# Kernel tuning notes

Measured on AMD Instinct MI355X. Metric: run time of the kernel, lower is better.

## Reference

```python
import jax, jax.numpy as jnp
import numpy as np

K = 3          # kernel size
KF = K * K     # kernel field = 9
PAD = 1
STRIDE = 1


def _conv(x, w, b):
    y = jax.lax.conv_general_dilated(
        x, w, (STRIDE, STRIDE), [(PAD, PAD), (PAD, PAD)],
        dimension_numbers=('NCHW', 'OIHW', 'NCHW'))
    return y + b[None, :, None, None]


def _bilinear_gather(x, py, px):
    # x: [B,C,H,W]; py/px: [B,KF,Ho,Wo] float sampling coords (zero-pad outside)
    B, C, H, W = x.shape
    xf = x.reshape(B, C, H * W)
    y0 = jnp.floor(py)
    x0 = jnp.floor(px)

    def corner(yc, xc):
        wy = 1.0 - jnp.abs(py - yc)
        wx = 1.0 - jnp.abs(px - xc)
        valid = (yc >= 0) & (yc <= H - 1) & (xc >= 0) & (xc <= W - 1)
        yi = jnp.clip(yc, 0, H - 1).astype(jnp.int32)
        xi = jnp.clip(xc, 0, W - 1).astype(jnp.int32)
        idx = (yi * W + xi).reshape(B, -1)               # [B, KF*Ho*Wo]
        v = jax.vmap(lambda f, i: f[:, i])(xf, idx)      # [B, C, KF*Ho*Wo]
        wgt = (wy * wx * valid.astype(x.dtype)).reshape(B, 1, -1)
        return v * wgt

    return (corner(y0, x0) + corner(y0, x0 + 1) +
            corner(y0 + 1, x0) + corner(y0 + 1, x0 + 1))  # [B,C,KF*Ho*Wo]


def _deform_conv(x, offset, mask, w, b):
    # modulated deformable conv v2 (mmcv offset layout: [y,x] interleaved per kernel pt)
    B, C, H, W = x.shape
    Ho, Wo = mask.shape[2], mask.shape[3]
    kh, kw = jnp.meshgrid(jnp.arange(K), jnp.arange(K), indexing='ij')
    kh = kh.reshape(-1).astype(x.dtype)   # [KF]
    kw = kw.reshape(-1).astype(x.dtype)
    base_y = (jnp.arange(Ho) * STRIDE - PAD).astype(x.dtype)
    base_x = (jnp.arange(Wo) * STRIDE - PAD).astype(x.dtype)
    off = offset.reshape(B, KF, 2, Ho, Wo)
    py = base_y[None, None, :, None] + kh[None, :, None, None] + off[:, :, 0]
    px = base_x[None, None, None, :] + kw[None, :, None, None] + off[:, :, 1]
    val = _bilinear_gather(x, py, px).reshape(B, C, KF, Ho, Wo)
    val = val * mask[:, None]                             # modulate
    out = jnp.einsum('bckhw,ock->bohw', val, w.reshape(w.shape[0], C, KF))
    return out + b[None, :, None, None]


def setup_inputs() -> dict:
    key = jax.random.key(0)
    k1, k2, k3 = jax.random.split(key, 3)
    B, C, H, W = 8, 64, 128, 128
    x = jax.random.normal(k1, (B, C, H, W), dtype=jnp.float32)
    w_om = jax.random.normal(k2, (3 * KF, C, K, K), dtype=jnp.float32) * 0.02
    b_om = jnp.zeros((3 * KF,), dtype=jnp.float32)
    w_dc = jax.random.normal(k3, (64, C, K, K), dtype=jnp.float32) * 0.05
    b_dc = jnp.zeros((64,), dtype=jnp.float32)
    return {"x": x, "w_om": w_om, "b_om": b_om, "w_dc": w_dc, "b_dc": b_dc}


def reference(x, w_om, b_om, w_dc, b_dc):
    om = _conv(x, w_om, b_om)                 # [B, 3*KF, H, W]
    offset = om[:, :2 * KF]
    mask = 2.0 * jax.nn.sigmoid(om[:, 2 * KF:])
    return _deform_conv(x, offset, mask, w_dc, b_dc)
```

## Files before the change

### kernel.cpp

```cpp
#include <hip/hip_runtime.h>
#include <cmath>

#define IH 128
#define IW 128
#define NB 8

typedef __attribute__((ext_vector_type(8))) short bf16x8;
typedef __attribute__((ext_vector_type(4))) float f32x4;

union U4B8 { uint4 u; bf16x8 h; };

#define XT_OFF   0
#define WTDC_OFF 4194304
#define WTOM_OFF (4194304 + 18432)

__device__ __forceinline__ unsigned short f32_to_bf16(float f) {
    unsigned int u = __float_as_uint(f);
    u += 0x7fffu + ((u >> 16) & 1u);
    return (unsigned short)(u >> 16);
}

__global__ void transpose_weights(const float* __restrict__ w_dc,
                                  const float* __restrict__ w_om,
                                  unsigned short* __restrict__ wt_dc16,
                                  unsigned short* __restrict__ wt_om16) {
    int idx = blockIdx.x * blockDim.x + threadIdx.x;
    if (idx < 9 * 64 * 64) {
        int k = idx >> 12;
        int o = (idx >> 6) & 63;
        int c = idx & 63;
        wt_dc16[idx] = f32_to_bf16(w_dc[(o * 64 + c) * 9 + k]);
    }
    if (idx < 9 * 32 * 64) {
        int k = idx >> 11;
        int o = (idx >> 6) & 31;
        int c = idx & 63;
        wt_om16[idx] = (o < 27) ? f32_to_bf16(w_om[(o * 64 + c) * 9 + k])
                                : (unsigned short)0;
    }
}

__global__ __launch_bounds__(256) void transpose_x(
        const float* __restrict__ x, unsigned short* __restrict__ xT) {
    __shared__ float t[64 * 65];
    const int tid = threadIdx.x;
    const int blk = blockIdx.x;
    const int b = blk >> 8;
    const int rem = blk & 255;
    const int h = rem >> 1;
    const int w0 = (rem & 1) << 6;

    for (int i = tid; i < 4096; i += 256) {
        const int c = i >> 6;
        const int w = i & 63;
        t[w * 65 + c] = x[(((size_t)(b * 64 + c)) << 14) + (h << 7) + w0 + w];
    }
    __syncthreads();
    const int c2 = (tid & 31) * 2;
    ushort2* dst = (ushort2*)(xT + (((size_t)b << 20)) + ((size_t)((h << 7) + w0)) * 64 + c2);
#pragma unroll
    for (int p = 0; p < 8; ++p) {
        const int w = (tid >> 5) + p * 8;
        ushort2 u;
        u.x = f32_to_bf16(t[w * 65 + c2]);
        u.y = f32_to_bf16(t[w * 65 + c2 + 1]);
        dst[(size_t)w * 32] = u;
    }
}

__device__ __forceinline__ void corner2(const unsigned short* __restrict__ p,
                                        float wgt, float* v) {
    const uint4 a = *(const uint4*)p;
    const uint4 c = *(const uint4*)(p + 32);
    unsigned int u[8] = {a.x, a.y, a.z, a.w, c.x, c.y, c.z, c.w};
#pragma unroll
    for (int i = 0; i < 8; ++i) {
        v[2 * i]     += wgt * __uint_as_float(u[i] << 16);
        v[2 * i + 1] += wgt * __uint_as_float(u[i] & 0xffff0000u);
    }
}

__global__ __launch_bounds__(256, 2) void fused_dcn(
        const unsigned short* __restrict__ xT,
        const float* __restrict__ b_om,
        const unsigned short* __restrict__ wt_om16,
        const float* __restrict__ b_dc,
        const unsigned short* __restrict__ wt_dc16,
        float* __restrict__ out) {
    __shared__ __align__(16) unsigned short wall[9 * 8 * 64 * 8];
    __shared__ __align__(16) float offs[27 * 68];

    const int tid = threadIdx.x;
    const int b = blockIdx.x >> 8;
    const int rem = blockIdx.x & 255;
    const int h = rem >> 1;
    const int w0 = (rem & 1) << 6;
    const int wid = tid >> 6;
    const int lane = tid & 63;
    const int ln15 = lane & 15;
    const int quad = lane >> 4;

    const unsigned short* xb = xT + ((size_t)b << 20);

    for (int s = tid; s < 2304; s += 256) {
        const int k = s >> 8;
        const int r = s & 255;
        const int p = r >> 5;
        const int o = r & 31;
        ((uint4*)wall)[s] = ((const uint4*)wt_om16)[(k << 8) + (o << 3) + p];
    }
    __syncthreads();

    {
        f32x4 acc[2] = {{0.f, 0.f, 0.f, 0.f}, {0.f, 0.f, 0.f, 0.f}};
#pragma unroll
        for (int k = 0; k < 9; ++k) {
            const int kh = k / 3;
            const int kw = k - kh * 3;
            const int y = h + kh - 1;
            const int xx = w0 + (wid << 4) + ln15 + kw - 1;
            U4B8 a0, a1;
            a0.u = make_uint4(0u, 0u, 0u, 0u);
            a1.u = make_uint4(0u, 0u, 0u, 0u);
            if (y >= 0 && y < IH && xx >= 0 && xx < IW) {
                const unsigned short* p = xb + (((size_t)((y << 7) + xx)) << 6) + (quad << 3);
                a0.u = *(const uint4*)p;
                a1.u = *(const uint4*)(p + 32);
            }
            const unsigned short* wb  = wall + (((k << 3) + quad) << 8);
            const unsigned short* wb4 = wall + (((k << 3) + quad + 4) << 8);
#pragma unroll
            for (int ot = 0; ot < 2; ++ot) {
                U4B8 b0, b1;
                b0.u = *(const uint4*)&wb [((ot << 4) + ln15) << 3];
                b1.u = *(const uint4*)&wb4[((ot << 4) + ln15) << 3];
                acc[ot] = __builtin_amdgcn_mfma_f32_16x16x32_bf16(a0.h, b0.h, acc[ot], 0, 0, 0);
                acc[ot] = __builtin_amdgcn_mfma_f32_16x16x32_bf16(a1.h, b1.h, acc[ot], 0, 0, 0);
            }
        }
#pragma unroll
        for (int ot = 0; ot < 2; ++ot) {
            const int o = (ot << 4) + ln15;
            if (o < 27) {
                const float bias = b_om[o];
                float4 r;
                r.x = acc[ot][0] + bias;
                r.y = acc[ot][1] + bias;
                r.z = acc[ot][2] + bias;
                r.w = acc[ot][3] + bias;
                if (o >= 18) {
                    r.x = 2.0f / (1.0f + __expf(-r.x));
                    r.y = 2.0f / (1.0f + __expf(-r.y));
                    r.z = 2.0f / (1.0f + __expf(-r.z));
                    r.w = 2.0f / (1.0f + __expf(-r.w));
                }
                *(float4*)&offs[o * 68 + (wid << 4) + (quad << 2)] = r;
            }
        }
    }
    __syncthreads();

    for (int s = tid; s < 4608; s += 256) {
        const int k = s >> 9;
        const int r = s & 511;
        const int p = r >> 6;
        const int o = r & 63;
        ((uint4*)wall)[s] = ((const uint4*)wt_dc16)[(k << 9) + (o << 3) + p];
    }
    __syncthreads();

    const int lpx = (wid << 4) + ln15;

    f32x4 acc[4];
#pragma unroll
    for (int i = 0; i < 4; ++i) acc[i] = (f32x4){0.f, 0.f, 0.f, 0.f};

#pragma unroll
    for (int k = 0; k < 9; ++k) {
        const float offy = offs[(2 * k) * 68 + lpx];
        const float offx = offs[(2 * k + 1) * 68 + lpx];
        const float msk  = offs[(18 + k) * 68 + lpx];
        const int kh = k / 3;
        const int kw = k - kh * 3;
        const float py  = (float)(h + kh - 1) + offy;
        const float pxf = (float)(w0 + lpx + kw - 1) + offx;
        const float y0f = floorf(py);
        const float x0f = floorf(pxf);
        const float fy = py - y0f;
        const float fx = pxf - x0f;
        const float wy0 = 1.0f - fy, wx0 = 1.0f - fx;
        const float vy0 = (y0f >= 0.0f && y0f <= 127.0f) ? 1.0f : 0.0f;
        const float vy1 = (y0f >= -1.0f && y0f <= 126.0f) ? 1.0f : 0.0f;
        const float vx0 = (x0f >= 0.0f && x0f <= 127.0f) ? 1.0f : 0.0f;
        const float vx1 = (x0f >= -1.0f && x0f <= 126.0f) ? 1.0f : 0.0f;
        const float w00 = wy0 * wx0 * vy0 * vx0;
        const float w01 = wy0 * fx  * vy0 * vx1;
        const float w10 = fy  * wx0 * vy1 * vx0;
        const float w11 = fy  * fx  * vy1 * vx1;
        const int y0i = min(max((int)y0f, 0), 127);
        const int y1i = min(max((int)y0f + 1, 0), 127);
        const int x0i = min(max((int)x0f, 0), 127);
        const int x1i = min(max((int)x0f + 1, 0), 127);

        float v[16];
#pragma unroll
        for (int i = 0; i < 16; ++i) v[i] = 0.0f;
        const int cofs = quad << 3;
        corner2(xb + ((((size_t)((y0i << 7) + x0i)) << 6) + cofs), w00, v);
        corner2(xb + ((((size_t)((y0i << 7) + x1i)) << 6) + cofs), w01, v);
        corner2(xb + ((((size_t)((y1i << 7) + x0i)) << 6) + cofs), w10, v);
        corner2(xb + ((((size_t)((y1i << 7) + x1i)) << 6) + cofs), w11, v);

        U4B8 a0, a1;
        unsigned int pk[8];
#pragma unroll
        for (int i = 0; i < 8; ++i) {
            const unsigned int lo = f32_to_bf16(v[2 * i] * msk);
            const unsigned int hi = f32_to_bf16(v[2 * i + 1] * msk);
            pk[i] = lo | (hi << 16);
        }
        a0.u = make_uint4(pk[0], pk[1], pk[2], pk[3]);
        a1.u = make_uint4(pk[4], pk[5], pk[6], pk[7]);

        const unsigned short* wb  = wall + (((k << 3) + quad) << 9);
        const unsigned short* wb4 = wall + (((k << 3) + quad + 4) << 9);
#pragma unroll
        for (int ot = 0; ot < 4; ++ot) {
            U4B8 b0, b1;
            b0.u = *(const uint4*)&wb [((ot << 4) + ln15) << 3];
            b1.u = *(const uint4*)&wb4[((ot << 4) + ln15) << 3];
            acc[ot] = __builtin_amdgcn_mfma_f32_16x16x32_bf16(a0.h, b0.h, acc[ot], 0, 0, 0);
            acc[ot] = __builtin_amdgcn_mfma_f32_16x16x32_bf16(a1.h, b1.h, acc[ot], 0, 0, 0);
        }
    }

#pragma unroll
    for (int ot = 0; ot < 4; ++ot) {
        const int o = (ot << 4) + ln15;
        const float bias = b_dc[o];
        float4 r;
        r.x = acc[ot][0] + bias;
        r.y = acc[ot][1] + bias;
        r.z = acc[ot][2] + bias;
        r.w = acc[ot][3] + bias;
        *(float4*)&out[(((size_t)(b * 64 + o)) << 14) + (h << 7) + w0 + (wid << 4) + (quad << 2)] = r;
    }
}

extern "C" void kernel_launch(void* const* d_in, const int* in_sizes, int n_in,
                              void* d_out, int out_size, void* d_ws, size_t ws_size,
                              hipStream_t stream) {
    const float* x    = (const float*)d_in[0];
    const float* w_om = (const float*)d_in[1];
    const float* b_om = (const float*)d_in[2];
    const float* w_dc = (const float*)d_in[3];
    const float* b_dc = (const float*)d_in[4];
    float* out = (float*)d_out;
    float* ws  = (float*)d_ws;

    unsigned short* xT      = (unsigned short*)(ws + XT_OFF);
    unsigned short* wt_dc16 = (unsigned short*)(ws + WTDC_OFF);
    unsigned short* wt_om16 = (unsigned short*)(ws + WTOM_OFF);

    const int n_blocks = NB * IH * (IW / 64);

    transpose_weights<<<144, 256, 0, stream>>>(w_dc, w_om, wt_dc16, wt_om16);
    transpose_x<<<NB * IH * 2, 256, 0, stream>>>(x, xT);
    fused_dcn<<<n_blocks, 256, 0, stream>>>(xT, b_om, wt_om16, b_dc, wt_dc16, out);
}
```

Measured before the change: 200.5 us.

## Switch to fp16 with packed bilinear FMA, double-buffered weights, merged prep kernel

Moves the activation and weight format from bf16 to fp16, so the bilinear corner accumulation can run as packed __hfma2 on half2 pairs with the mask folded into the corner weights, replacing the scalar fp32 unpack and bf16 repack. Per-tap weight slices are now streamed into a small double-buffered LDS area instead of staging all nine taps at once. Together with raising launch bounds to four blocks per CU, this is meant to increase occupancy. The two preprocessing kernels are merged into one launch. In exchange it adds a block barrier per kernel tap, and fp16 accumulation of the interpolated values is less precise than fp32.

```diff
diff --git a/kernel.cpp b/kernel.cpp
--- a/kernel.cpp
+++ b/kernel.cpp
@@ -1,93 +1,70 @@
 #include <hip/hip_runtime.h>
+#include <hip/hip_fp16.h>
 #include <cmath>
 
 #define IH 128
 #define IW 128
 #define NB 8
 
-typedef __attribute__((ext_vector_type(8))) short bf16x8;
+typedef __attribute__((ext_vector_type(8))) _Float16 f16x8;
 typedef __attribute__((ext_vector_type(4))) float f32x4;
 
-union U4B8 { uint4 u; bf16x8 h; };
+union U4H8 { uint4 u; f16x8 h; __half2 h2[4]; };
 
 #define XT_OFF   0
 #define WTDC_OFF 4194304
 #define WTOM_OFF (4194304 + 18432)
 
-__device__ __forceinline__ unsigned short f32_to_bf16(float f) {
-    unsigned int u = __float_as_uint(f);
-    u += 0x7fffu + ((u >> 16) & 1u);
-    return (unsigned short)(u >> 16);
-}
-
-__global__ void transpose_weights(const float* __restrict__ w_dc,
-                                  const float* __restrict__ w_om,
-                                  unsigned short* __restrict__ wt_dc16,
-                                  unsigned short* __restrict__ wt_om16) {
-    int idx = blockIdx.x * blockDim.x + threadIdx.x;
-    if (idx < 9 * 64 * 64) {
-        int k = idx >> 12;
-        int o = (idx >> 6) & 63;
-        int c = idx & 63;
-        wt_dc16[idx] = f32_to_bf16(w_dc[(o * 64 + c) * 9 + k]);
-    }
-    if (idx < 9 * 32 * 64) {
-        int k = idx >> 11;
-        int o = (idx >> 6) & 31;
-        int c = idx & 63;
-        wt_om16[idx] = (o < 27) ? f32_to_bf16(w_om[(o * 64 + c) * 9 + k])
-                                : (unsigned short)0;
-    }
-}
-
-__global__ __launch_bounds__(256) void transpose_x(
-        const float* __restrict__ x, unsigned short* __restrict__ xT) {
-    __shared__ float t[64 * 65];
+__global__ __launch_bounds__(256) void prep(
+        const float* __restrict__ x,
+        const float* __restrict__ w_dc,
+        const float* __restrict__ w_om,
+        __half* __restrict__ xT,
+        __half* __restrict__ wt_dc16,
+        __half* __restrict__ wt_om16) {
     const int tid = threadIdx.x;
     const int blk = blockIdx.x;
-    const int b = blk >> 8;
-    const int rem = blk & 255;
-    const int h = rem >> 1;
-    const int w0 = (rem & 1) << 6;
-
-    for (int i = tid; i < 4096; i += 256) {
-        const int c = i >> 6;
-        const int w = i & 63;
-        t[w * 65 + c] = x[(((size_t)(b * 64 + c)) << 14) + (h << 7) + w0 + w];
-    }
-    __syncthreads();
-    const int c2 = (tid & 31) * 2;
-    ushort2* dst = (ushort2*)(xT + (((size_t)b << 20)) + ((size_t)((h << 7) + w0)) * 64 + c2);
-#pragma unroll
-    for (int p = 0; p < 8; ++p) {
-        const int w = (tid >> 5) + p * 8;
-        ushort2 u;
-        u.x = f32_to_bf16(t[w * 65 + c2]);
-        u.y = f32_to_bf16(t[w * 65 + c2 + 1]);
-        dst[(size_t)w * 32] = u;
+    if (blk < 2048) {
+        __shared__ float t[64 * 65];
+        const int b = blk >> 8;
+        const int rem = blk & 255;
+        const int h = rem >> 1;
+        const int w0 = (rem & 1) << 6;
+        for (int i = tid; i < 4096; i += 256) {
+            const int c = i >> 6;
+            const int w = i & 63;
+            t[w * 65 + c] = x[(((size_t)(b * 64 + c)) << 14) + (h << 7) + w0 + w];
+        }
+        __syncthreads();
+        const int c2 = (tid & 31) * 2;
+        __half2* dst = (__half2*)(xT + (((size_t)b << 20)) + ((size_t)((h << 7) + w0)) * 64 + c2);
+#pragma unroll
+        for (int p = 0; p < 8; ++p) {
+            const int w = (tid >> 5) + p * 8;
+            dst[(size_t)w * 32] = __floats2half2_rn(t[w * 65 + c2], t[w * 65 + c2 + 1]);
+        }
+    } else {
+        const int base = (blk - 2048) * 256 + tid;
+        for (int idx = base; idx < 9 * 64 * 64; idx += 2048) {
+            const int k = idx >> 12, o = (idx >> 6) & 63, c = idx & 63;
+            wt_dc16[idx] = __float2half_rn(w_dc[(o * 64 + c) * 9 + k]);
+        }
+        for (int idx = base; idx < 9 * 32 * 64; idx += 2048) {
+            const int k = idx >> 11, o = (idx >> 6) & 31, c = idx & 63;
+            wt_om16[idx] = (o < 27) ? __float2half_rn(w_om[(o * 64 + c) * 9 + k])
+                                    : __float2half_rn(0.0f);
+        }
     }
 }
 
-__device__ __forceinline__ void corner2(const unsigned short* __restrict__ p,
-                                        float wgt, float* v) {
-    const uint4 a = *(const uint4*)p;
-    const uint4 c = *(const uint4*)(p + 32);
-    unsigned int u[8] = {a.x, a.y, a.z, a.w, c.x, c.y, c.z, c.w};
-#pragma unroll
-    for (int i = 0; i < 8; ++i) {
-        v[2 * i]     += wgt * __uint_as_float(u[i] << 16);
-        v[2 * i + 1] += wgt * __uint_as_float(u[i] & 0xffff0000u);
-    }
-}
-
-__global__ __launch_bounds__(256, 2) void fused_dcn(
-        const unsigned short* __restrict__ xT,
+__global__ __launch_bounds__(256, 4) void fused_dcn(
+        const __half* __restrict__ xT,
         const float* __restrict__ b_om,
-        const unsigned short* __restrict__ wt_om16,
+        const __half* __restrict__ wt_om16,
         const float* __restrict__ b_dc,
-        const unsigned short* __restrict__ wt_dc16,
+        const __half* __restrict__ wt_dc16,
         float* __restrict__ out) {
-    __shared__ __align__(16) unsigned short wall[9 * 8 * 64 * 8];
+    __shared__ __align__(16) __half wk[2][8 * 64 * 8];
     __shared__ __align__(16) float offs[27 * 68];
 
     const int tid = threadIdx.x;
@@ -99,15 +76,13 @@
     const int lane = tid & 63;
     const int ln15 = lane & 15;
     const int quad = lane >> 4;
-
-    const unsigned short* xb = xT + ((size_t)b << 20);
-
-    for (int s = tid; s < 2304; s += 256) {
-        const int k = s >> 8;
-        const int r = s & 255;
-        const int p = r >> 5;
-        const int o = r & 31;
-        ((uint4*)wall)[s] = ((const uint4*)wt_om16)[(k << 8) + (o << 3) + p];
+    const int lpx = (wid << 4) + ln15;
+
+    const __half* xb = xT + ((size_t)b << 20);
+
+    {
+        const int p = tid >> 5, o = tid & 31;
+        ((uint4*)wk[0])[tid] = ((const uint4*)wt_om16)[(o << 3) + p];
     }
     __syncthreads();
 
@@ -115,28 +90,33 @@
         f32x4 acc[2] = {{0.f, 0.f, 0.f, 0.f}, {0.f, 0.f, 0.f, 0.f}};
 #pragma unroll
         for (int k = 0; k < 9; ++k) {
+            if (k < 8) {
+                const int p = tid >> 5, o = tid & 31;
+                ((uint4*)wk[(k & 1) ^ 1])[tid] =
+                    ((const uint4*)wt_om16)[((k + 1) << 8) + (o << 3) + p];
+            }
             const int kh = k / 3;
             const int kw = k - kh * 3;
             const int y = h + kh - 1;
-            const int xx = w0 + (wid << 4) + ln15 + kw - 1;
-            U4B8 a0, a1;
+            const int xx = w0 + lpx + kw - 1;
+            U4H8 a0, a1;
             a0.u = make_uint4(0u, 0u, 0u, 0u);
             a1.u = make_uint4(0u, 0u, 0u, 0u);
             if (y >= 0 && y < IH && xx >= 0 && xx < IW) {
-                const unsigned short* p = xb + (((size_t)((y << 7) + xx)) << 6) + (quad << 3);
+                const __half* p = xb + (((size_t)((y << 7) + xx)) << 6) + (quad << 3);
                 a0.u = *(const uint4*)p;
                 a1.u = *(const uint4*)(p + 32);
             }
-            const unsigned short* wb  = wall + (((k << 3) + quad) << 8);
-            const unsigned short* wb4 = wall + (((k << 3) + quad + 4) << 8);
+            const __half* wb = wk[k & 1];
 #pragma unroll
             for (int ot = 0; ot < 2; ++ot) {
-                U4B8 b0, b1;
-                b0.u = *(const uint4*)&wb [((ot << 4) + ln15) << 3];
-                b1.u = *(const uint4*)&wb4[((ot << 4) + ln15) << 3];
-                acc[ot] = __builtin_amdgcn_mfma_f32_16x16x32_bf16(a0.h, b0.h, acc[ot], 0, 0, 0);
-                acc[ot] = __builtin_amdgcn_mfma_f32_16x16x32_bf16(a1.h, b1.h, acc[ot], 0, 0, 0);
-            }
+                U4H8 b0, b1;
+                b0.u = *(const uint4*)&wb[((quad << 5) + (ot << 4) + ln15) << 3];
+                b1.u = *(const uint4*)&wb[(((quad + 4) << 5) + (ot << 4) + ln15) << 3];
+                acc[ot] = __builtin_amdgcn_mfma_f32_16x16x32_f16(a0.h, b0.h, acc[ot], 0, 0, 0);
+                acc[ot] = __builtin_amdgcn_mfma_f32_16x16x32_f16(a1.h, b1.h, acc[ot], 0, 0, 0);
+            }
+            if (k < 8) __syncthreads();
         }
 #pragma unroll
         for (int ot = 0; ot < 2; ++ot) {
@@ -160,23 +140,25 @@
     }
     __syncthreads();
 
-    for (int s = tid; s < 4608; s += 256) {
-        const int k = s >> 9;
-        const int r = s & 511;
-        const int p = r >> 6;
-        const int o = r & 63;
-        ((uint4*)wall)[s] = ((const uint4*)wt_dc16)[(k << 9) + (o << 3) + p];
+    for (int s = tid; s < 512; s += 256) {
+        const int p = s >> 6, o = s & 63;
+        ((uint4*)wk[0])[s] = ((const uint4*)wt_dc16)[(o << 3) + p];
     }
     __syncthreads();
 
-    const int lpx = (wid << 4) + ln15;
-
     f32x4 acc[4];
 #pragma unroll
     for (int i = 0; i < 4; ++i) acc[i] = (f32x4){0.f, 0.f, 0.f, 0.f};
 
 #pragma unroll
     for (int k = 0; k < 9; ++k) {
+        if (k < 8) {
+            for (int s = tid; s < 512; s += 256) {
+                const int p = s >> 6, o = s & 63;
+                ((uint4*)wk[(k & 1) ^ 1])[s] =
+                    ((const uint4*)wt_dc16)[((k + 1) << 9) + (o << 3) + p];
+            }
+        }
         const float offy = offs[(2 * k) * 68 + lpx];
         const float offx = offs[(2 * k + 1) * 68 + lpx];
         const float msk  = offs[(18 + k) * 68 + lpx];
@@ -193,45 +175,57 @@
         const float vy1 = (y0f >= -1.0f && y0f <= 126.0f) ? 1.0f : 0.0f;
         const float vx0 = (x0f >= 0.0f && x0f <= 127.0f) ? 1.0f : 0.0f;
         const float vx1 = (x0f >= -1.0f && x0f <= 126.0f) ? 1.0f : 0.0f;
-        const float w00 = wy0 * wx0 * vy0 * vx0;
-        const float w01 = wy0 * fx  * vy0 * vx1;
-        const float w10 = fy  * wx0 * vy1 * vx0;
-        const float w11 = fy  * fx  * vy1 * vx1;
+        const __half2 W00 = __float2half2_rn(wy0 * wx0 * vy0 * vx0 * msk);
+        const __half2 W01 = __float2half2_rn(wy0 * fx  * vy0 * vx1 * msk);
+        const __half2 W10 = __float2half2_rn(fy  * wx0 * vy1 * vx0 * msk);
+        const __half2 W11 = __float2half2_rn(fy  * fx  * vy1 * vx1 * msk);
         const int y0i = min(max((int)y0f, 0), 127);
         const int y1i = min(max((int)y0f + 1, 0), 127);
         const int x0i = min(max((int)x0f, 0), 127);
         const int x1i = min(max((int)x0f + 1, 0), 127);
 
-        float v[16];
-#pragma unroll
-        for (int i = 0; i < 16; ++i) v[i] = 0.0f;
+        const __half2 hz = __float2half2_rn(0.0f);
+        __half2 v[8] = {hz, hz, hz, hz, hz, hz, hz, hz};
         const int cofs = quad << 3;
-        corner2(xb + ((((size_t)((y0i << 7) + x0i)) << 6) + cofs), w00, v);
-        corner2(xb + ((((size_t)((y0i << 7) + x1i)) << 6) + cofs), w01, v);
-        corner2(xb + ((((size_t)((y1i << 7) + x0i)) << 6) + cofs), w10, v);
-        corner2(xb + ((((size_t)((y1i << 7) + x1i)) << 6) + cofs), w11, v);
-
-        U4B8 a0, a1;
-        unsigned int pk[8];
-#pragma unroll
-        for (int i = 0; i < 8; ++i) {
-            const unsigned int lo = f32_to_bf16(v[2 * i] * msk);
-            const unsigned int hi = f32_to_bf16(v[2 * i + 1] * msk);
-            pk[i] = lo | (hi << 16);
-        }
-        a0.u = make_uint4(pk[0], pk[1], pk[2], pk[3]);
-        a1.u = make_uint4(pk[4], pk[5], pk[6], pk[7]);
-
-        const unsigned short* wb  = wall + (((k << 3) + quad) << 9);
-        const unsigned short* wb4 = wall + (((k << 3) + quad + 4) << 9);
+        {
+            const __half* p = xb + (((size_t)((y0i << 7) + x0i)) << 6) + cofs;
+            U4H8 ca, cb; ca.u = *(const uint4*)p; cb.u = *(const uint4*)(p + 32);
+#pragma unroll
+            for (int i = 0; i < 4; ++i) { v[i] = __hfma2(ca.h2[i], W00, v[i]); v[4 + i] = __hfma2(cb.h2[i], W00, v[4 + i]); }
+        }
+        {
+            const __half* p = xb + (((size_t)((y0i << 7) + x1i)) << 6) + cofs;
+            U4H8 ca, cb; ca.u = *(const uint4*)p; cb.u = *(const uint4*)(p + 32);
+#pragma unroll
+            for (int i = 0; i < 4; ++i) { v[i] = __hfma2(ca.h2[i], W01, v[i]); v[4 + i] = __hfma2(cb.h2[i], W01, v[4 + i]); }
+        }
+        {
+            const __half* p = xb + (((size_t)((y1i << 7) + x0i)) << 6) + cofs;
+            U4H8 ca, cb; ca.u = *(const uint4*)p; cb.u = *(const uint4*)(p + 32);
+#pragma unroll
+            for (int i = 0; i < 4; ++i) { v[i] = __hfma2(ca.h2[i], W10, v[i]); v[4 + i] = __hfma2(cb.h2[i], W10, v[4 + i]); }
+        }
+        {
+            const __half* p = xb + (((size_t)((y1i << 7) + x1i)) << 6) + cofs;
+            U4H8 ca, cb; ca.u = *(const uint4*)p; cb.u = *(const uint4*)(p + 32);
+#pragma unroll
+            for (int i = 0; i < 4; ++i) { v[i] = __hfma2(ca.h2[i], W11, v[i]); v[4 + i] = __hfma2(cb.h2[i], W11, v[4 + i]); }
+        }
+
+        U4H8 a0, a1;
+#pragma unroll
+        for (int i = 0; i < 4; ++i) { a0.h2[i] = v[i]; a1.h2[i] = v[4 + i]; }
+
+        const __half* wb = wk[k & 1];
 #pragma unroll
         for (int ot = 0; ot < 4; ++ot) {
-            U4B8 b0, b1;
-            b0.u = *(const uint4*)&wb [((ot << 4) + ln15) << 3];
-            b1.u = *(const uint4*)&wb4[((ot << 4) + ln15) << 3];
-            acc[ot] = __builtin_amdgcn_mfma_f32_16x16x32_bf16(a0.h, b0.h, acc[ot], 0, 0, 0);
-            acc[ot] = __builtin_amdgcn_mfma_f32_16x16x32_bf16(a1.h, b1.h, acc[ot], 0, 0, 0);
-        }
+            U4H8 b0, b1;
+            b0.u = *(const uint4*)&wb[((quad << 6) + (ot << 4) + ln15) << 3];
+            b1.u = *(const uint4*)&wb[(((quad + 4) << 6) + (ot << 4) + ln15) << 3];
+            acc[ot] = __builtin_amdgcn_mfma_f32_16x16x32_f16(a0.h, b0.h, acc[ot], 0, 0, 0);
+            acc[ot] = __builtin_amdgcn_mfma_f32_16x16x32_f16(a1.h, b1.h, acc[ot], 0, 0, 0);
+        }
+        if (k < 8) __syncthreads();
     }
 
 #pragma unroll
@@ -258,13 +252,10 @@
     float* out = (float*)d_out;
     float* ws  = (float*)d_ws;
 
-    unsigned short* xT      = (unsigned short*)(ws + XT_OFF);
-    unsigned short* wt_dc16 = (unsigned short*)(ws + WTDC_OFF);
-    unsigned short* wt_om16 = (unsigned short*)(ws + WTOM_OFF);
-
-    const int n_blocks = NB * IH * (IW / 64);
-
-    transpose_weights<<<144, 256, 0, stream>>>(w_dc, w_om, wt_dc16, wt_om16);
-    transpose_x<<<NB * IH * 2, 256, 0, stream>>>(x, xT);
-    fused_dcn<<<n_blocks, 256, 0, stream>>>(xT, b_om, wt_om16, b_dc, wt_dc16, out);
+    __half* xT      = (__half*)(ws + XT_OFF);
+    __half* wt_dc16 = (__half*)(ws + WTDC_OFF);
+    __half* wt_om16 = (__half*)(ws + WTOM_OFF);
+
+    prep<<<2056, 256, 0, stream>>>(x, w_dc, w_om, xT, wt_dc16, wt_om16);
+    fused_dcn<<<NB * IH * (IW / 64), 256, 0, stream>>>(xT, b_om, wt_om16, b_dc, wt_dc16, out);
 }
```

Result: slower. 205.3 us (+2.4%).
